# Optimization experiments

Hardware: AMD Instinct MI355X
Metric: run time of the kernel (lower is better)

The kernel has to match this reference:

```python
import jax, jax.numpy as jnp
import numpy as np

NUM_GRAPHS = 64


def setup_inputs() -> dict:
    key = jax.random.key(0)
    ks = jax.random.split(key, 8)
    N, E, D_IN, D_H = 50000, 800000, 128, 256
    x = jax.random.uniform(ks[0], (N, D_IN), dtype=jnp.float32)
    edge_index = jax.random.randint(ks[1], (2, E), 0, N, dtype=jnp.int64)
    batch = jnp.sort(jax.random.randint(ks[2], (N,), 0, NUM_GRAPHS, dtype=jnp.int64))
    s = 1.0 / np.sqrt(D_IN)
    s2 = 1.0 / np.sqrt(D_H)
    W1_rel = jax.random.normal(ks[3], (D_IN, D_H), dtype=jnp.float32) * s
    W1_root = jax.random.normal(ks[4], (D_IN, D_H), dtype=jnp.float32) * s
    b1 = jnp.zeros((D_H,), jnp.float32)
    W2_rel = jax.random.normal(ks[5], (D_H, D_H), dtype=jnp.float32) * s2
    W2_root = jax.random.normal(ks[6], (D_H, D_H), dtype=jnp.float32) * s2
    b2 = jnp.zeros((D_H,), jnp.float32)
    return {"x": x, "edge_index": edge_index, "batch": batch,
            "W1_rel": W1_rel, "W1_root": W1_root, "b1": b1,
            "W2_rel": W2_rel, "W2_root": W2_root, "b2": b2}


def reference(x, edge_index, batch, W1_rel, W1_root, b1, W2_rel, W2_root, b2):
    N = x.shape[0]
    src, dst = edge_index[0], edge_index[1]

    # handcrafted features: per-label fraction of total feature mass + log(graph_size)
    graph_size = jnp.sum(x)
    handcrafted = jnp.concatenate([jnp.sum(x, axis=0) / graph_size,
                                   jnp.log(graph_size)[None]])

    def graph_conv(h, W_rel, W_root, b):
        # PyG GraphConv (aggr='add'): out_i = W_rel @ sum_{j->i} h_j + W_root @ h_i + b
        agg = jax.ops.segment_sum(h[src], dst, num_segments=N)  # [N, d]
        return agg @ W_rel + h @ W_root + b

    h = jax.nn.relu(graph_conv(x, W1_rel, W1_root, b1))
    # layers 2..num_layers share the same weights (module instance reused in original)
    for _ in range(2):
        h = jax.nn.relu(graph_conv(h, W2_rel, W2_root, b2))

    # global_mean_pool over batch ids
    counts = jax.ops.segment_sum(jnp.ones((N,), h.dtype), batch, num_segments=NUM_GRAPHS)
    pooled = jax.ops.segment_sum(h, batch, num_segments=NUM_GRAPHS)
    pooled = pooled / jnp.maximum(counts, 1.0)[:, None]
    return pooled, handcrafted
```

## Files before the change

### kernel.cpp

```cpp
#include <hip/hip_runtime.h>
#include <hip/hip_bf16.h>
#include <string.h>

#define NN 50000
#define NE 800000
#define DIN 128
#define DH 256
#define NG 64
#define PSPLIT 32

typedef short bf16x8 __attribute__((ext_vector_type(8)));
typedef float f32x4 __attribute__((ext_vector_type(4)));

__device__ __forceinline__ float bf2f(__hip_bfloat16 v) { return __bfloat162float(v); }
__device__ __forceinline__ float bfbits(unsigned int lo16) {
  unsigned int u = lo16 << 16;
  float f;
  memcpy(&f, &u, 4);
  return f;
}
__device__ __forceinline__ unsigned int packbf2(float x, float y) {
  __hip_bfloat16 bx = __float2bfloat16(x), by = __float2bfloat16(y);
  unsigned short ux, uy;
  memcpy(&ux, &bx, 2);
  memcpy(&uy, &by, 2);
  return (unsigned int)ux | ((unsigned int)uy << 16);
}

__device__ __forceinline__ float loadF(const void* p, long i, int fbf) {
  return fbf ? bf2f(((const __hip_bfloat16*)p)[i]) : ((const float*)p)[i];
}
__device__ __forceinline__ void storeF(void* p, long i, float v, int fbf) {
  if (fbf) ((__hip_bfloat16*)p)[i] = __float2bfloat16(v);
  else ((float*)p)[i] = v;
}
__device__ __forceinline__ int loadI(const void* p, long i, int i64) {
  return i64 ? (int)((const long long*)p)[i] : ((const int*)p)[i];
}

__device__ __forceinline__ int lb_batch(const void* batch, int i64, int target) {
  int lo = 0, hi = NN;
  while (lo < hi) {
    int mid = (lo + hi) >> 1;
    if (loadI(batch, mid, i64) < target) lo = mid + 1;
    else hi = mid;
  }
  return lo;
}

__global__ void k_detect(const void* x, const void* ei, int* flags) {
  __shared__ int s_f32sig, s_i32sig;
  if (threadIdx.x == 0) { s_f32sig = 0; s_i32sig = 0; }
  __syncthreads();
  int t = threadIdx.x;
  const unsigned short* u = (const unsigned short*)x;
  int f = 0;
  for (int i = 2 * t; i < 8192; i += 512) if (u[i] >= 0x4000) f = 1;
  const unsigned int* w = (const unsigned int*)ei;
  int g = 0;
  for (int i = 2 * t + 1; i < 8192; i += 512) if (w[i] != 0u) g = 1;
  if (f) atomicOr(&s_f32sig, 1);
  if (g) atomicOr(&s_i32sig, 1);
  __syncthreads();
  if (t == 0) { flags[0] = s_f32sig ? 0 : 1; flags[1] = s_i32sig ? 0 : 1; }
}

__global__ void k_zero(int* __restrict__ p, int n) {
  int i = blockIdx.x * blockDim.x + threadIdx.x;
  int stride = gridDim.x * blockDim.x;
  for (; i < n; i += stride) p[i] = 0;
}

__global__ __launch_bounds__(256) void k_prep(
    const void* __restrict__ x, __hip_bfloat16* __restrict__ xb,
    float* __restrict__ colsum, const int* __restrict__ flags) {
  int fbf = flags[0];
  int t = threadIdx.x;
  int lane16 = t & 15;
  int rowoff = t >> 4;
  float acc[8] = {};
  for (int r = blockIdx.x * 16 + rowoff; r < NN; r += gridDim.x * 16) {
    uint4 o;
    if (fbf) {
      uint4 v = ((const uint4*)x)[(long)r * 16 + lane16];
      acc[0] += bfbits(v.x & 0xffffu); acc[1] += bfbits(v.x >> 16);
      acc[2] += bfbits(v.y & 0xffffu); acc[3] += bfbits(v.y >> 16);
      acc[4] += bfbits(v.z & 0xffffu); acc[5] += bfbits(v.z >> 16);
      acc[6] += bfbits(v.w & 0xffffu); acc[7] += bfbits(v.w >> 16);
      o = v;
    } else {
      float4 a = ((const float4*)x)[(long)r * 32 + lane16 * 2];
      float4 b = ((const float4*)x)[(long)r * 32 + lane16 * 2 + 1];
      acc[0] += a.x; acc[1] += a.y; acc[2] += a.z; acc[3] += a.w;
      acc[4] += b.x; acc[5] += b.y; acc[6] += b.z; acc[7] += b.w;
      o.x = packbf2(a.x, a.y); o.y = packbf2(a.z, a.w);
      o.z = packbf2(b.x, b.y); o.w = packbf2(b.z, b.w);
    }
    ((uint4*)xb)[((long)(lane16 >> 2) * NN + r) * 4 + (lane16 & 3)] = o;
  }
  __shared__ float s[16][DIN];
#pragma unroll
  for (int k = 0; k < 8; ++k) s[rowoff][lane16 * 8 + k] = acc[k];
  __syncthreads();
  if (t < DIN) {
    float v = 0.f;
#pragma unroll
    for (int ro = 0; ro < 16; ++ro) v += s[ro][t];
    atomicAdd(&colsum[t], v);
  }
}

__global__ void k_handcrafted(const float* __restrict__ colsum, void* __restrict__ out,
                              const int* __restrict__ flags) {
  __shared__ float s[DIN];
  int fbf = flags[0];
  int t = threadIdx.x;
  s[t] = colsum[t];
  __syncthreads();
  for (int off = DIN / 2; off > 0; off >>= 1) {
    if (t < off) s[t] += s[t + off];
    __syncthreads();
  }
  float g = s[0];
  storeF(out, NG * DH + t, colsum[t] / g, fbf);
  if (t == 0) storeF(out, NG * DH + DIN, logf(g), fbf);
}

__global__ void k_pack_w(const void* __restrict__ Wrel, const void* __restrict__ Wroot,
                         const void* __restrict__ bias, __hip_bfloat16* __restrict__ pack,
                         float* __restrict__ biasf, const int* __restrict__ flags, int K) {
  int fbf = flags[0];
  int KS = K >> 5;
  int total = 2 * K * DH;
  int i = blockIdx.x * blockDim.x + threadIdx.x;
  int stride = gridDim.x * blockDim.x;
  for (int p = i; p < total; p += stride) {
    int m = p / (K * DH);
    int r = p % (K * DH);
    int j = r & 7;
    int l = (r >> 3) & 63;
    int q2 = r >> 9;
    int ks = q2 % KS;
    int ct = q2 / KS;
    int kk = ks * 32 + (l >> 4) * 8 + j;
    int col = ct * 16 + (l & 15);
    const void* W = m ? Wroot : Wrel;
    pack[p] = __float2bfloat16(loadF(W, (long)kk * DH + col, fbf));
  }
  if (i < DH) biasf[i] = loadF(bias, i, fbf);
}

__global__ void k_deg(const void* __restrict__ ei, int* __restrict__ cnt,
                      const int* __restrict__ flags) {
  int i64 = flags[1];
  int e = blockIdx.x * blockDim.x + threadIdx.x;
  int stride = gridDim.x * blockDim.x;
  for (; e < NE; e += stride) {
    int d = loadI(ei, (long)NE + e, i64);
    d = min(max(d, 0), NN - 1);
    atomicAdd(&cnt[d], 1);
  }
}

#define SCAN_B 256
__global__ void k_scan1(const int* __restrict__ cnt, int* __restrict__ rowptr,
                        int* __restrict__ bsum) {
  __shared__ int s[SCAN_B];
  int b = blockIdx.x, t = threadIdx.x;
  int i = b * SCAN_B + t;
  int v = (i < NN) ? cnt[i] : 0;
  s[t] = v;
  __syncthreads();
  for (int off = 1; off < SCAN_B; off <<= 1) {
    int xv = (t >= off) ? s[t - off] : 0;
    __syncthreads();
    s[t] += xv;
    __syncthreads();
  }
  if (i < NN) rowptr[i] = s[t] - v;
  if (t == SCAN_B - 1) bsum[b] = s[t];
}

__global__ void k_scan2(int* __restrict__ bsum, int nb) {
  __shared__ int s[SCAN_B];
  int t = threadIdx.x;
  int v = (t < nb) ? bsum[t] : 0;
  s[t] = v;
  __syncthreads();
  for (int off = 1; off < SCAN_B; off <<= 1) {
    int xv = (t >= off) ? s[t - off] : 0;
    __syncthreads();
    s[t] += xv;
    __syncthreads();
  }
  if (t < nb) bsum[t] = s[t] - v;
}

__global__ void k_scan3(int* __restrict__ rowptr, const int* __restrict__ bsum) {
  int i = blockIdx.x * blockDim.x + threadIdx.x;
  int stride = gridDim.x * blockDim.x;
  for (; i < NN; i += stride) rowptr[i] += bsum[i >> 8];
  if (blockIdx.x == 0 && threadIdx.x == 0) rowptr[NN] = NE;
}

__global__ void k_fill(const void* __restrict__ ei, const int* __restrict__ rowptr,
                       int* __restrict__ cur, int* __restrict__ srcs,
                       const int* __restrict__ flags) {
  int i64 = flags[1];
  int e = blockIdx.x * blockDim.x + threadIdx.x;
  int stride = gridDim.x * blockDim.x;
  for (; e < NE; e += stride) {
    int s = loadI(ei, e, i64);
    int d = loadI(ei, (long)NE + e, i64);
    s = min(max(s, 0), NN - 1);
    d = min(max(d, 0), NN - 1);
    int p = atomicAdd(&cur[d], 1);
    srcs[rowptr[d] + p] = s;
  }
}

template <int LOG>
__global__ __launch_bounds__(256) void k_gather(
    const int* __restrict__ rowptr, const int* __restrict__ srcs,
    const __hip_bfloat16* __restrict__ hs, __hip_bfloat16* __restrict__ aggs) {
  int b = blockIdx.x;
  int slice = b & ((1 << LOG) - 1);
  int tile = b >> LOG;
  int lane = threadIdx.x & 63;
  int wave = threadIdx.x >> 6;
  int slot = lane >> 3;
  int cu = lane & 7;
  int node = tile * 32 + wave * 8 + slot;
  if (node > NN - 1) node = NN - 1;
  int beg = rowptr[node], end = rowptr[node + 1];
  const uint2* hsl = (const uint2*)hs + (size_t)slice * NN * 8;
  float a0 = 0.f, a1 = 0.f, a2 = 0.f, a3 = 0.f;
  int i = beg;
  for (; i + 7 < end; i += 8) {
    uint2 v[8];
#pragma unroll
    for (int u = 0; u < 8; ++u) {
      int sv = __builtin_nontemporal_load(srcs + i + u);
      v[u] = hsl[sv * 8 + cu];
    }
#pragma unroll
    for (int u = 0; u < 8; ++u) {
      a0 += bfbits(v[u].x & 0xffffu);
      a1 += bfbits(v[u].x >> 16);
      a2 += bfbits(v[u].y & 0xffffu);
      a3 += bfbits(v[u].y >> 16);
    }
  }
  for (; i < end; ++i) {
    int sv = __builtin_nontemporal_load(srcs + i);
    uint2 v0 = hsl[sv * 8 + cu];
    a0 += bfbits(v0.x & 0xffffu);
    a1 += bfbits(v0.x >> 16);
    a2 += bfbits(v0.y & 0xffffu);
    a3 += bfbits(v0.y >> 16);
  }
  unsigned int* ap = (unsigned int*)aggs + (size_t)slice * NN * 16;
  __builtin_nontemporal_store(packbf2(a0, a1), ap + node * 16 + cu * 2);
  __builtin_nontemporal_store(packbf2(a2, a3), ap + node * 16 + cu * 2 + 1);
}

template <int K>
__global__ __launch_bounds__(256, 4) void k_gemm(
    const __hip_bfloat16* __restrict__ A1, const __hip_bfloat16* __restrict__ A2,
    const __hip_bfloat16* __restrict__ Wpack, const float* __restrict__ bias,
    __hip_bfloat16* __restrict__ out) {
  constexpr int KS = K >> 5;
  int lane = threadIdx.x & 63;
  int wave = threadIdx.x >> 6;
  int m15 = lane & 15;
  int q = lane >> 4;
  int row0 = blockIdx.x * 32;
  const short* A1s = (const short*)A1;
  const short* A2s = (const short*)A2;
  const short* Wp = (const short*)Wpack;
  const int wrootOfs = K * DH;
  f32x4 acc[2][4] = {};
#pragma unroll
  for (int ks = 0; ks < KS; ++ks) {
    bf16x8 a1[2], a2[2], b1[4], b2[4];
#pragma unroll
    for (int mt = 0; mt < 2; ++mt) {
      int r = row0 + mt * 16 + m15;
      if (r > NN - 1) r = NN - 1;
      long ad = ((long)ks * NN + r) * 32 + q * 8;
      a1[mt] = *(const bf16x8*)(A1s + ad);
      a2[mt] = *(const bf16x8*)(A2s + ad);
    }
#pragma unroll
    for (int ct = 0; ct < 4; ++ct) {
      int gct = wave * 4 + ct;
      const short* base = Wp + ((gct * KS + ks) * 64 + lane) * 8;
      b1[ct] = *(const bf16x8*)(base);
      b2[ct] = *(const bf16x8*)(base + wrootOfs);
    }
#pragma unroll
    for (int mt = 0; mt < 2; ++mt)
#pragma unroll
      for (int ct = 0; ct < 4; ++ct) {
        acc[mt][ct] = __builtin_amdgcn_mfma_f32_16x16x32_bf16(a1[mt], b1[ct], acc[mt][ct], 0, 0, 0);
        acc[mt][ct] = __builtin_amdgcn_mfma_f32_16x16x32_bf16(a2[mt], b2[ct], acc[mt][ct], 0, 0, 0);
      }
  }
#pragma unroll
  for (int mt = 0; mt < 2; ++mt)
#pragma unroll
    for (int ct = 0; ct < 4; ++ct) {
      int col = (wave * 4 + ct) * 16 + m15;
      float bv = bias[col];
      int slice = col >> 5, cof = col & 31;
#pragma unroll
      for (int r = 0; r < 4; ++r) {
        int row = row0 + mt * 16 + q * 4 + r;
        if (row < NN) {
          float v = acc[mt][ct][r] + bv;
          out[((long)slice * NN + row) * 32 + cof] = __float2bfloat16(fmaxf(v, 0.f));
        }
      }
    }
}

__global__ void k_poolpart(const void* __restrict__ batch, const __hip_bfloat16* __restrict__ h,
                           float* __restrict__ pooled, const int* __restrict__ flags) {
  int i64 = flags[1];
  int g = blockIdx.x;
  int p = blockIdx.y;
  int j = threadIdx.x;
  int s = lb_batch(batch, i64, g);
  int e = lb_batch(batch, i64, g + 1);
  int len = e - s;
  if (len <= 0) return;
  int chunk = (len + PSPLIT - 1) / PSPLIT;
  int rs = s + p * chunk;
  int re = min(rs + chunk, e);
  if (rs >= re) return;
  const unsigned int* h2 = (const unsigned int*)h;
  int slice = j >> 4, cu = j & 15;
  float a0 = 0.f, a1 = 0.f;
  for (int r = rs; r < re; ++r) {
    unsigned int v = h2[((long)slice * NN + r) * 16 + cu];
    a0 += bfbits(v & 0xffffu);
    a1 += bfbits(v >> 16);
  }
  atomicAdd(&pooled[g * DH + 2 * j], a0);
  atomicAdd(&pooled[g * DH + 2 * j + 1], a1);
}

__global__ void k_poolfin(const void* __restrict__ batch, const float* __restrict__ pooled,
                          void* __restrict__ out, const int* __restrict__ flags) {
  int fbf = flags[0];
  int i64 = flags[1];
  int g = blockIdx.x;
  int j = threadIdx.x;
  int s = lb_batch(batch, i64, g);
  int e = lb_batch(batch, i64, g + 1);
  float cnt = fmaxf((float)(e - s), 1.0f);
  storeF(out, (long)g * DH + j, pooled[g * DH + j] / cnt, fbf);
}

extern "C" void kernel_launch(void* const* d_in, const int* in_sizes, int n_in,
                              void* d_out, int out_size, void* d_ws, size_t ws_size,
                              hipStream_t stream) {
  const void* x = d_in[0];
  const void* ei = d_in[1];
  const void* batch = d_in[2];
  const void* W1r = d_in[3];
  const void* W1o = d_in[4];
  const void* b1 = d_in[5];
  const void* W2r = d_in[6];
  const void* W2o = d_in[7];
  const void* b2 = d_in[8];
  void* out = d_out;

  char* w = (char*)d_ws;
  auto alloc = [&](size_t bytes) -> char* {
    char* p = w;
    w += (bytes + 255) & ~(size_t)255;
    return p;
  };
  int* flags = (int*)alloc(64);
  const int zero_n = NN + NN + DIN + NG * DH;
  int* zreg = (int*)alloc((size_t)zero_n * 4);
  int* cnt = zreg;
  int* cur = cnt + NN;
  float* colsum = (float*)(cur + NN);
  float* pooled = (float*)(colsum + DIN);
  int* rowptr = (int*)alloc((NN + 1) * 4);
  int* bsum = (int*)alloc(SCAN_B * 4);
  int* srcs = (int*)alloc((size_t)NE * 4);
  __hip_bfloat16* xb = (__hip_bfloat16*)alloc((size_t)NN * DIN * 2);
  __hip_bfloat16* aggb = (__hip_bfloat16*)alloc((size_t)NN * DH * 2);
  __hip_bfloat16* hA = (__hip_bfloat16*)alloc((size_t)NN * DH * 2);
  __hip_bfloat16* hB = (__hip_bfloat16*)alloc((size_t)NN * DH * 2);
  __hip_bfloat16* wp1 = (__hip_bfloat16*)alloc((size_t)2 * DIN * DH * 2);
  __hip_bfloat16* wp2 = (__hip_bfloat16*)alloc((size_t)2 * DH * DH * 2);
  float* b1f = (float*)alloc(DH * 4);
  float* b2f = (float*)alloc(DH * 4);

  const int nblk = (NN + SCAN_B - 1) / SCAN_B;
  const int gemm_grid = (NN + 31) / 32;
  const int ntiles = (NN + 31) / 32;
  const int gat256_grid = ntiles * 8;
  const int gat128_grid = ntiles * 4;

  k_detect<<<1, 256, 0, stream>>>(x, ei, flags);
  k_zero<<<512, 256, 0, stream>>>(zreg, zero_n);

  k_pack_w<<<64, 256, 0, stream>>>(W1r, W1o, b1, wp1, b1f, flags, DIN);
  k_pack_w<<<128, 256, 0, stream>>>(W2r, W2o, b2, wp2, b2f, flags, DH);
  k_prep<<<1024, 256, 0, stream>>>(x, xb, colsum, flags);
  k_handcrafted<<<1, 128, 0, stream>>>(colsum, out, flags);

  k_deg<<<1024, 256, 0, stream>>>(ei, cnt, flags);
  k_scan1<<<nblk, SCAN_B, 0, stream>>>(cnt, rowptr, bsum);
  k_scan2<<<1, SCAN_B, 0, stream>>>(bsum, nblk);
  k_scan3<<<256, 256, 0, stream>>>(rowptr, bsum);
  k_fill<<<1024, 256, 0, stream>>>(ei, rowptr, cur, srcs, flags);

  k_gather<2><<<gat128_grid, 256, 0, stream>>>(rowptr, srcs, xb, aggb);
  k_gemm<DIN><<<gemm_grid, 256, 0, stream>>>(aggb, xb, wp1, b1f, hA);
  k_gather<3><<<gat256_grid, 256, 0, stream>>>(rowptr, srcs, hA, aggb);
  k_gemm<DH><<<gemm_grid, 256, 0, stream>>>(aggb, hA, wp2, b2f, hB);
  k_gather<3><<<gat256_grid, 256, 0, stream>>>(rowptr, srcs, hB, aggb);
  k_gemm<DH><<<gemm_grid, 256, 0, stream>>>(aggb, hB, wp2, b2f, hA);

  k_poolpart<<<dim3(NG, PSPLIT), 128, 0, stream>>>(batch, hA, pooled, flags);
  k_poolfin<<<NG, DH, 0, stream>>>(batch, pooled, out, flags);
}
```

Before: 590.8 us.

## Sort nodes by in-degree to balance gather waves; simplify bf16 unpacking

```diff
diff --git a/kernel.cpp b/kernel.cpp
--- a/kernel.cpp
+++ b/kernel.cpp
@@ -15,6 +15,11 @@
 __device__ __forceinline__ float bf2f(__hip_bfloat16 v) { return __bfloat162float(v); }
 __device__ __forceinline__ float bfbits(unsigned int lo16) {
   unsigned int u = lo16 << 16;
+  float f;
+  memcpy(&f, &u, 4);
+  return f;
+}
+__device__ __forceinline__ float asf(unsigned int u) {
   float f;
   memcpy(&f, &u, 4);
   return f;
@@ -219,9 +224,39 @@
   }
 }
 
+__global__ void k_hist(const int* __restrict__ cnt, int* __restrict__ bins) {
+  int n = blockIdx.x * blockDim.x + threadIdx.x;
+  if (n < NN) atomicAdd(&bins[min(cnt[n], 255)], 1);
+}
+
+__global__ void k_binscan(int* __restrict__ bins) {
+  __shared__ int s[256];
+  int t = threadIdx.x;
+  int v = bins[t];
+  s[t] = v;
+  __syncthreads();
+  for (int off = 1; off < 256; off <<= 1) {
+    int xv = (t >= off) ? s[t - off] : 0;
+    __syncthreads();
+    s[t] += xv;
+    __syncthreads();
+  }
+  bins[t] = s[t] - v;
+}
+
+__global__ void k_order(const int* __restrict__ cnt, int* __restrict__ bins,
+                        int* __restrict__ order) {
+  int n = blockIdx.x * blockDim.x + threadIdx.x;
+  if (n < NN) {
+    int pos = atomicAdd(&bins[min(cnt[n], 255)], 1);
+    order[pos] = n;
+  }
+}
+
 template <int LOG>
 __global__ __launch_bounds__(256) void k_gather(
     const int* __restrict__ rowptr, const int* __restrict__ srcs,
+    const int* __restrict__ order,
     const __hip_bfloat16* __restrict__ hs, __hip_bfloat16* __restrict__ aggs) {
   int b = blockIdx.x;
   int slice = b & ((1 << LOG) - 1);
@@ -230,8 +265,9 @@
   int wave = threadIdx.x >> 6;
   int slot = lane >> 3;
   int cu = lane & 7;
-  int node = tile * 32 + wave * 8 + slot;
-  if (node > NN - 1) node = NN - 1;
+  int gnode = tile * 32 + wave * 8 + slot;
+  if (gnode > NN - 1) gnode = NN - 1;
+  int node = order[gnode];
   int beg = rowptr[node], end = rowptr[node + 1];
   const uint2* hsl = (const uint2*)hs + (size_t)slice * NN * 8;
   float a0 = 0.f, a1 = 0.f, a2 = 0.f, a3 = 0.f;
@@ -245,19 +281,19 @@
     }
 #pragma unroll
     for (int u = 0; u < 8; ++u) {
-      a0 += bfbits(v[u].x & 0xffffu);
-      a1 += bfbits(v[u].x >> 16);
-      a2 += bfbits(v[u].y & 0xffffu);
-      a3 += bfbits(v[u].y >> 16);
+      a0 += asf(v[u].x << 16);
+      a1 += asf(v[u].x & 0xFFFF0000u);
+      a2 += asf(v[u].y << 16);
+      a3 += asf(v[u].y & 0xFFFF0000u);
     }
   }
   for (; i < end; ++i) {
     int sv = __builtin_nontemporal_load(srcs + i);
     uint2 v0 = hsl[sv * 8 + cu];
-    a0 += bfbits(v0.x & 0xffffu);
-    a1 += bfbits(v0.x >> 16);
-    a2 += bfbits(v0.y & 0xffffu);
-    a3 += bfbits(v0.y >> 16);
+    a0 += asf(v0.x << 16);
+    a1 += asf(v0.x & 0xFFFF0000u);
+    a2 += asf(v0.y << 16);
+    a3 += asf(v0.y & 0xFFFF0000u);
   }
   unsigned int* ap = (unsigned int*)aggs + (size_t)slice * NN * 16;
   __builtin_nontemporal_store(packbf2(a0, a1), ap + node * 16 + cu * 2);
@@ -383,14 +419,16 @@
     return p;
   };
   int* flags = (int*)alloc(64);
-  const int zero_n = NN + NN + DIN + NG * DH;
+  const int zero_n = NN + NN + 256 + DIN + NG * DH;
   int* zreg = (int*)alloc((size_t)zero_n * 4);
   int* cnt = zreg;
   int* cur = cnt + NN;
-  float* colsum = (float*)(cur + NN);
+  int* bins = cur + NN;
+  float* colsum = (float*)(bins + 256);
   float* pooled = (float*)(colsum + DIN);
   int* rowptr = (int*)alloc((NN + 1) * 4);
   int* bsum = (int*)alloc(SCAN_B * 4);
+  int* order = (int*)alloc(NN * 4);
   int* srcs = (int*)alloc((size_t)NE * 4);
   __hip_bfloat16* xb = (__hip_bfloat16*)alloc((size_t)NN * DIN * 2);
   __hip_bfloat16* aggb = (__hip_bfloat16*)alloc((size_t)NN * DH * 2);
@@ -421,11 +459,15 @@
   k_scan3<<<256, 256, 0, stream>>>(rowptr, bsum);
   k_fill<<<1024, 256, 0, stream>>>(ei, rowptr, cur, srcs, flags);
 
-  k_gather<2><<<gat128_grid, 256, 0, stream>>>(rowptr, srcs, xb, aggb);
+  k_hist<<<nblk, 256, 0, stream>>>(cnt, bins);
+  k_binscan<<<1, 256, 0, stream>>>(bins);
+  k_order<<<nblk, 256, 0, stream>>>(cnt, bins, order);
+
+  k_gather<2><<<gat128_grid, 256, 0, stream>>>(rowptr, srcs, order, xb, aggb);
   k_gemm<DIN><<<gemm_grid, 256, 0, stream>>>(aggb, xb, wp1, b1f, hA);
-  k_gather<3><<<gat256_grid, 256, 0, stream>>>(rowptr, srcs, hA, aggb);
+  k_gather<3><<<gat256_grid, 256, 0, stream>>>(rowptr, srcs, order, hA, aggb);
   k_gemm<DH><<<gemm_grid, 256, 0, stream>>>(aggb, hA, wp2, b2f, hB);
-  k_gather<3><<<gat256_grid, 256, 0, stream>>>(rowptr, srcs, hB, aggb);
+  k_gather<3><<<gat256_grid, 256, 0, stream>>>(rowptr, srcs, order, hB, aggb);
   k_gemm<DH><<<gemm_grid, 256, 0, stream>>>(aggb, hB, wp2, b2f, hA);
 
   k_poolpart<<<dim3(NG, PSPLIT), 128, 0, stream>>>(batch, hA, pooled, flags);
```

Result: slower. 887.0 us (+50.1%).
